# Kernel optimization log

Measured on AMD Instinct MI355X. Metric: run time of the kernel, lower is better.

## Reference

```python
import jax, jax.numpy as jnp
import numpy as np

DIM = 1024

def setup_inputs() -> dict:
    key = jax.random.key(0)
    k1, k2, k3, k4 = jax.random.split(key, 4)
    x = jax.random.normal(k1, (4, 4096, DIM), dtype=jnp.float32)
    A = jax.random.normal(k2, (DIM, DIM), dtype=jnp.float32) * 0.01
    B_w = jax.random.normal(k3, (DIM, DIM), dtype=jnp.float32) * (1.0 / np.sqrt(DIM))
    C_w = jax.random.normal(k4, (DIM, DIM), dtype=jnp.float32) * (1.0 / np.sqrt(DIM))
    D = jnp.ones((DIM,), dtype=jnp.float32)
    return {"x": x, "A": A, "B_w": B_w, "C_w": C_w, "D": D}

def reference(x, A, B_w, C_w, D):
    # x: [B, L, Dm]; recurrence: h_t = tanh(h_{t-1} @ A.T + x_t @ B_w.T)
    #                 y_t = h_t @ C_w.T + D * x_t
    Bsz, L, Dm = x.shape
    # Precompute the input projection for all steps at once (one big GEMM).
    bx = jnp.einsum('bld,ed->ble', x, B_w)  # [B, L, Dm]

    def step(h, inputs):
        bx_t, x_t = inputs
        h = jnp.tanh(h @ A.T + bx_t)
        y = h @ C_w.T + D * x_t
        return h, y

    h0 = jnp.zeros((Bsz, Dm), dtype=x.dtype)
    # scan over time axis: move L to leading dim
    _, ys = jax.lax.scan(step, h0, (jnp.swapaxes(bx, 0, 1), jnp.swapaxes(x, 0, 1)))
    return jnp.swapaxes(ys, 0, 1)  # [B, L, Dm]
```

## Files before the change

kernel.cpp:

```cpp
#include <hip/hip_runtime.h>
#include <math.h>

#define DM   1024
#define BSZ  4
#define LSEQ 4096
#define GPB  32
#define RPW  32
#define NSEG 8
#define CPS  128
#define TPB  256

typedef unsigned long long u64;

__global__ __launch_bounds__(TPB) void bx_gemm_kernel(
    const float* __restrict__ X, const float* __restrict__ Bw,
    float* __restrict__ out)
{
    __shared__ float xs[16][68];
    __shared__ float bs[16][68];
    const int bm = blockIdx.x, bn = blockIdx.y;
    const int t  = threadIdx.x;
    const int tx = t & 15, ty = t >> 4;
    const int ml = t >> 2;
    const int kq = (t & 3) * 4;
    const float* xg = X  + (size_t)(bm * 64 + ml) * DM + kq;
    const float* bg = Bw + (size_t)(bn * 64 + ml) * DM + kq;
    float acc[4][4] = {};
    for (int k0 = 0; k0 < DM; k0 += 16) {
        float4 xv = *(const float4*)(xg + k0);
        float4 bv = *(const float4*)(bg + k0);
        __syncthreads();
        xs[kq+0][ml] = xv.x; xs[kq+1][ml] = xv.y; xs[kq+2][ml] = xv.z; xs[kq+3][ml] = xv.w;
        bs[kq+0][ml] = bv.x; bs[kq+1][ml] = bv.y; bs[kq+2][ml] = bv.z; bs[kq+3][ml] = bv.w;
        __syncthreads();
        #pragma unroll
        for (int kk = 0; kk < 16; ++kk) {
            float a[4], c[4];
            #pragma unroll
            for (int i = 0; i < 4; ++i) a[i] = xs[kk][ty*4+i];
            #pragma unroll
            for (int j = 0; j < 4; ++j) c[j] = bs[kk][tx*4+j];
            #pragma unroll
            for (int i = 0; i < 4; ++i)
                #pragma unroll
                for (int j = 0; j < 4; ++j)
                    acc[i][j] += a[i] * c[j];
        }
    }
    #pragma unroll
    for (int i = 0; i < 4; ++i) {
        float4 v = make_float4(acc[i][0], acc[i][1], acc[i][2], acc[i][3]);
        *(float4*)(out + (size_t)(bm*64 + ty*4 + i)*DM + bn*64 + tx*4) = v;
    }
}

__global__ __launch_bounds__(TPB, 1) void scan_kernel(
    const float* __restrict__ A, const float* __restrict__ Cw,
    const float* __restrict__ Dv, const float* __restrict__ X,
    float* __restrict__ Y, u64* hbuf)
{
    __shared__ float hs[DM];
    __shared__ float pA[NSEG][RPW + 1];
    __shared__ float pC[NSEG][RPW + 1];
    const int b   = blockIdx.x >> 5;
    const int gw  = blockIdx.x & 31;
    const int r0  = gw * RPW;
    const int t   = threadIdx.x;
    const int r   = t & 31;
    const int seg = t >> 5;

    float ra[CPS], rc[CPS];
    {
        const float* Ap = A  + (size_t)(r0 + r) * DM + seg * CPS;
        const float* Cp = Cw + (size_t)(r0 + r) * DM + seg * CPS;
        #pragma unroll
        for (int u = 0; u < CPS / 4; ++u) {
            float4 v = *(const float4*)(Ap + u*4);
            ra[u*4+0]=v.x; ra[u*4+1]=v.y; ra[u*4+2]=v.z; ra[u*4+3]=v.w;
            float4 w = *(const float4*)(Cp + u*4);
            rc[u*4+0]=w.x; rc[u*4+1]=w.y; rc[u*4+2]=w.z; rc[u*4+3]=w.w;
        }
    }
    const float dv = Dv[r0 + (t & 31)];

    for (int k = 0; k <= LSEQ; ++k) {
        u64* src = hbuf + (size_t)(k & 1) * BSZ * DM + (size_t)b * DM;
        u64 v0 = __hip_atomic_load(src + t,       __ATOMIC_RELAXED, __HIP_MEMORY_SCOPE_AGENT);
        u64 v1 = __hip_atomic_load(src + t + 256, __ATOMIC_RELAXED, __HIP_MEMORY_SCOPE_AGENT);
        u64 v2 = __hip_atomic_load(src + t + 512, __ATOMIC_RELAXED, __HIP_MEMORY_SCOPE_AGENT);
        u64 v3 = __hip_atomic_load(src + t + 768, __ATOMIC_RELAXED, __HIP_MEMORY_SCOPE_AGENT);
        const unsigned tag = (unsigned)k;
        int spins = 0;
        while ((((unsigned)(v0 >> 32)) != tag || ((unsigned)(v1 >> 32)) != tag ||
                ((unsigned)(v2 >> 32)) != tag || ((unsigned)(v3 >> 32)) != tag)
               && ++spins < (1 << 20)) {
            if ((unsigned)(v0 >> 32) != tag)
                v0 = __hip_atomic_load(src + t,       __ATOMIC_RELAXED, __HIP_MEMORY_SCOPE_AGENT);
            if ((unsigned)(v1 >> 32) != tag)
                v1 = __hip_atomic_load(src + t + 256, __ATOMIC_RELAXED, __HIP_MEMORY_SCOPE_AGENT);
            if ((unsigned)(v2 >> 32) != tag)
                v2 = __hip_atomic_load(src + t + 512, __ATOMIC_RELAXED, __HIP_MEMORY_SCOPE_AGENT);
            if ((unsigned)(v3 >> 32) != tag)
                v3 = __hip_atomic_load(src + t + 768, __ATOMIC_RELAXED, __HIP_MEMORY_SCOPE_AGENT);
        }
        hs[t]       = __uint_as_float((unsigned)v0);
        hs[t + 256] = __uint_as_float((unsigned)v1);
        hs[t + 512] = __uint_as_float((unsigned)v2);
        hs[t + 768] = __uint_as_float((unsigned)v3);
        __syncthreads();

        float accA = 0.f, accC = 0.f;
        const float4* h4p = (const float4*)(hs + seg * CPS);
        #pragma unroll
        for (int u = 0; u < CPS / 4; ++u) {
            float4 h4 = h4p[u];
            accA += ra[u*4+0]*h4.x + ra[u*4+1]*h4.y + ra[u*4+2]*h4.z + ra[u*4+3]*h4.w;
            accC += rc[u*4+0]*h4.x + rc[u*4+1]*h4.y + rc[u*4+2]*h4.z + rc[u*4+3]*h4.w;
        }
        pA[seg][r] = accA;
        pC[seg][r] = accC;
        __syncthreads();

        if (t < RPW) {
            float sA = 0.f, sC = 0.f;
            #pragma unroll
            for (int s = 0; s < NSEG; ++s) { sA += pA[s][t]; sC += pC[s][t]; }
            if (k < LSEQ) {
                const size_t bxoff = (size_t)b*LSEQ*DM + (size_t)k*DM + r0 + t;
                float hv = tanhf(sA + Y[bxoff]);
                u64 pk = ((u64)(unsigned)(k + 1) << 32) | (u64)__float_as_uint(hv);
                __hip_atomic_store(hbuf + (size_t)((k+1) & 1) * BSZ * DM + (size_t)b * DM + r0 + t,
                                   pk, __ATOMIC_RELAXED, __HIP_MEMORY_SCOPE_AGENT);
            }
            if (k > 0) {
                const size_t yoff = (size_t)b*LSEQ*DM + (size_t)(k-1)*DM + r0 + t;
                Y[yoff] = sC + dv * X[yoff];
            }
        }
    }
}

extern "C" void kernel_launch(void* const* d_in, const int* in_sizes, int n_in,
                              void* d_out, int out_size, void* d_ws, size_t ws_size,
                              hipStream_t stream)
{
    const float* X  = (const float*)d_in[0];
    const float* A  = (const float*)d_in[1];
    const float* Bw = (const float*)d_in[2];
    const float* Cw = (const float*)d_in[3];
    const float* Dv = (const float*)d_in[4];
    float* Y   = (float*)d_out;
    u64* hbuf  = (u64*)d_ws;

    hipMemsetAsync(d_ws, 0, (size_t)2 * BSZ * DM * sizeof(u64), stream);

    dim3 g1((BSZ * LSEQ) / 64, DM / 64);
    bx_gemm_kernel<<<g1, TPB, 0, stream>>>(X, Bw, Y);
    scan_kernel<<<BSZ * GPB, TPB, 0, stream>>>(A, Cw, Dv, X, Y, hbuf);
}
```

Before: 12.96 ms.

## Reduce scan critical path with shuffle reductions and deferred Cw output projection

The scan kernel now maps 8 lanes per row and reduces the A·h partial sums with wave shuffles instead of an LDS partial-sum array plus a second barrier. The hidden state is published as soon as the A product finishes. The Cw rows move from registers into padded LDS, and the output projection is computed after the store, off the inter-block critical path. The bx value is prefetched before the spin-wait. The kernel needs about 139KB of dynamic LDS and reads C from LDS every step; a trailing barrier is added per step.

```diff
diff --git a/kernel.cpp b/kernel.cpp
--- a/kernel.cpp
+++ b/kernel.cpp
@@ -6,9 +6,10 @@
 #define LSEQ 4096
 #define GPB  32
 #define RPW  32
-#define NSEG 8
-#define CPS  128
 #define TPB  256
+#define SP   132
+#define HSW  1056
+#define RS   1056
 
 typedef unsigned long long u64;
 
@@ -59,31 +60,41 @@
     const float* __restrict__ Dv, const float* __restrict__ X,
     float* __restrict__ Y, u64* hbuf)
 {
-    __shared__ float hs[DM];
-    __shared__ float pA[NSEG][RPW + 1];
-    __shared__ float pC[NSEG][RPW + 1];
+    extern __shared__ float lds[];
+    float* cs = lds;
+    float* hs = lds + RPW * RS;
     const int b   = blockIdx.x >> 5;
     const int gw  = blockIdx.x & 31;
     const int r0  = gw * RPW;
     const int t   = threadIdx.x;
-    const int r   = t & 31;
-    const int seg = t >> 5;
+    const int row = t >> 3;
+    const int seg = t & 7;
+    const bool lead = (seg == 0);
 
-    float ra[CPS], rc[CPS];
+    float ra[128];
     {
-        const float* Ap = A  + (size_t)(r0 + r) * DM + seg * CPS;
-        const float* Cp = Cw + (size_t)(r0 + r) * DM + seg * CPS;
+        const float* Ap = A + (size_t)(r0 + row) * DM + seg * 128;
         #pragma unroll
-        for (int u = 0; u < CPS / 4; ++u) {
+        for (int u = 0; u < 32; ++u) {
             float4 v = *(const float4*)(Ap + u*4);
             ra[u*4+0]=v.x; ra[u*4+1]=v.y; ra[u*4+2]=v.z; ra[u*4+3]=v.w;
-            float4 w = *(const float4*)(Cp + u*4);
-            rc[u*4+0]=w.x; rc[u*4+1]=w.y; rc[u*4+2]=w.z; rc[u*4+3]=w.w;
         }
     }
-    const float dv = Dv[r0 + (t & 31)];
+    for (int i = 0; i < 32; ++i) {
+        int idx = i * TPB + t;
+        int rr  = idx >> 8;
+        int c   = (idx & 255) * 4;
+        float4 v = *(const float4*)(Cw + (size_t)(r0 + rr) * DM + c);
+        *(float4*)(cs + rr * RS + (c >> 7) * SP + (c & 127)) = v;
+    }
+    const float dv = Dv[r0 + row];
+    __syncthreads();
 
     for (int k = 0; k <= LSEQ; ++k) {
+        float bxv = 0.f;
+        if (lead && k < LSEQ)
+            bxv = Y[(size_t)b*LSEQ*DM + (size_t)k*DM + r0 + row];
+
         u64* src = hbuf + (size_t)(k & 1) * BSZ * DM + (size_t)b * DM;
         u64 v0 = __hip_atomic_load(src + t,       __ATOMIC_RELAXED, __HIP_MEMORY_SCOPE_AGENT);
         u64 v1 = __hip_atomic_load(src + t + 256, __ATOMIC_RELAXED, __HIP_MEMORY_SCOPE_AGENT);
@@ -103,40 +114,53 @@
             if ((unsigned)(v3 >> 32) != tag)
                 v3 = __hip_atomic_load(src + t + 768, __ATOMIC_RELAXED, __HIP_MEMORY_SCOPE_AGENT);
         }
-        hs[t]       = __uint_as_float((unsigned)v0);
-        hs[t + 256] = __uint_as_float((unsigned)v1);
-        hs[t + 512] = __uint_as_float((unsigned)v2);
-        hs[t + 768] = __uint_as_float((unsigned)v3);
+        {
+            int c0 = t, c1 = t + 256, c2 = t + 512, c3 = t + 768;
+            hs[(c0 >> 7) * SP + (c0 & 127)] = __uint_as_float((unsigned)v0);
+            hs[(c1 >> 7) * SP + (c1 & 127)] = __uint_as_float((unsigned)v1);
+            hs[(c2 >> 7) * SP + (c2 & 127)] = __uint_as_float((unsigned)v2);
+            hs[(c3 >> 7) * SP + (c3 & 127)] = __uint_as_float((unsigned)v3);
+        }
         __syncthreads();
 
-        float accA = 0.f, accC = 0.f;
-        const float4* h4p = (const float4*)(hs + seg * CPS);
-        #pragma unroll
-        for (int u = 0; u < CPS / 4; ++u) {
-            float4 h4 = h4p[u];
-            accA += ra[u*4+0]*h4.x + ra[u*4+1]*h4.y + ra[u*4+2]*h4.z + ra[u*4+3]*h4.w;
-            accC += rc[u*4+0]*h4.x + rc[u*4+1]*h4.y + rc[u*4+2]*h4.z + rc[u*4+3]*h4.w;
-        }
-        pA[seg][r] = accA;
-        pC[seg][r] = accC;
-        __syncthreads();
-
-        if (t < RPW) {
-            float sA = 0.f, sC = 0.f;
+        float accA = 0.f;
+        {
+            const float4* h4p = (const float4*)(hs + seg * SP);
             #pragma unroll
-            for (int s = 0; s < NSEG; ++s) { sA += pA[s][t]; sC += pC[s][t]; }
-            if (k < LSEQ) {
-                const size_t bxoff = (size_t)b*LSEQ*DM + (size_t)k*DM + r0 + t;
-                float hv = tanhf(sA + Y[bxoff]);
-                u64 pk = ((u64)(unsigned)(k + 1) << 32) | (u64)__float_as_uint(hv);
-                __hip_atomic_store(hbuf + (size_t)((k+1) & 1) * BSZ * DM + (size_t)b * DM + r0 + t,
-                                   pk, __ATOMIC_RELAXED, __HIP_MEMORY_SCOPE_AGENT);
-            }
-            if (k > 0) {
-                const size_t yoff = (size_t)b*LSEQ*DM + (size_t)(k-1)*DM + r0 + t;
-                Y[yoff] = sC + dv * X[yoff];
+            for (int u = 0; u < 32; ++u) {
+                float4 h4 = h4p[u];
+                accA += ra[u*4+0]*h4.x + ra[u*4+1]*h4.y + ra[u*4+2]*h4.z + ra[u*4+3]*h4.w;
             }
         }
+        accA += __shfl_xor(accA, 1);
+        accA += __shfl_xor(accA, 2);
+        accA += __shfl_xor(accA, 4);
+        if (lead && k < LSEQ) {
+            float hv = tanhf(accA + bxv);
+            u64 pk = ((u64)(unsigned)(k + 1) << 32) | (u64)__float_as_uint(hv);
+            __hip_atomic_store(hbuf + (size_t)((k+1) & 1) * BSZ * DM + (size_t)b * DM + r0 + row,
+                               pk, __ATOMIC_RELAXED, __HIP_MEMORY_SCOPE_AGENT);
+        }
+
+        if (k > 0) {
+            float accC = 0.f;
+            const float4* c4p = (const float4*)(cs + row * RS + seg * SP);
+            const float4* h4p = (const float4*)(hs + seg * SP);
+            #pragma unroll
+            for (int u = 0; u < 32; ++u) {
+                float4 c4 = c4p[u];
+                float4 h4 = h4p[u];
+                accC += c4.x*h4.x + c4.y*h4.y + c4.z*h4.z + c4.w*h4.w;
+            }
+            accC += __shfl_xor(accC, 1);
+            accC += __shfl_xor(accC, 2);
+            accC += __shfl_xor(accC, 4);
+            if (lead) {
+                const size_t yoff = (size_t)b*LSEQ*DM + (size_t)(k-1)*DM + r0 + row;
+                Y[yoff] = accC + dv * X[yoff];
+            }
+        }
+        __syncthreads();
     }
 }
 
@@ -156,5 +180,6 @@
 
     dim3 g1((BSZ * LSEQ) / 64, DM / 64);
     bx_gemm_kernel<<<g1, TPB, 0, stream>>>(X, Bw, Y);
-    scan_kernel<<<BSZ * GPB, TPB, 0, stream>>>(A, Cw, Dv, X, Y, hbuf);
+    const size_t lds_bytes = (size_t)(RPW * RS + HSW) * sizeof(float);
+    scan_kernel<<<BSZ * GPB, TPB, lds_bytes, stream>>>(A, Cw, Dv, X, Y, hbuf);
 }
```

Result: faster. 11.51 ms (-11.2%).
